# Performance work log

Hardware: AMD Instinct MI355X
Metric: run time of the kernel (lower is better)

The kernel has to match this reference:

```python
import jax, jax.numpy as jnp
import numpy as np

N = 8192
D = 256  # hidden_size = in_features = out_features
NEG_SLOPE = 0.01  # nn.LeakyReLU() default
MASK_VAL = -1e12


def setup_inputs() -> dict:
    key = jax.random.key(0)
    k1, k2, k3, k4 = jax.random.split(key, 4)
    x = jax.random.normal(k1, (N, D), dtype=jnp.float32)
    adj = jax.random.randint(k2, (N, N), 0, 2, dtype=jnp.int32)
    # kaiming_uniform_ style params (scaled random uniform)
    W = jax.random.normal(k3, (D, D), dtype=jnp.float32) * (1.0 / np.sqrt(D))
    a = jax.random.normal(k4, (2 * D, 1), dtype=jnp.float32) * (1.0 / np.sqrt(2 * D))
    return {"x": x, "adj": adj, "W": W, "a": a}


def reference(x, adj, W, a):
    # GraphAttentionLayer.forward (eval mode: dropout is identity)
    h = x @ W  # [N, D]
    # a_input[i,j] = concat(h_i, h_j); a_input @ a decomposes as:
    #   e[i,j] = h_i . a[:D] + h_j . a[D:]
    # identical math without materializing the [N, N, 2D] tensor.
    e_src = h @ a[:D, 0]  # [N]
    e_dst = h @ a[D:, 0]  # [N]
    e = e_src[:, None] + e_dst[None, :]  # [N, N]
    e = jnp.where(e > 0, e, NEG_SLOPE * e)  # LeakyReLU
    att_logits = jnp.where(adj > 0, e, MASK_VAL)
    attention = jax.nn.softmax(att_logits, axis=1)
    h_prime = attention @ h  # [N, D]
    return jax.nn.elu(h_prime)  # concat=True branch
```

## Files before the change

kernel.cpp:

```cpp
#include <hip/hip_runtime.h>

#define NN 8192
#define DD 256
#define JSPLIT 2
#define JCH (NN / JSPLIT)
#define NSTEP (JCH / 32)

typedef __attribute__((ext_vector_type(8))) short short8;
typedef __attribute__((ext_vector_type(4))) float f32x4;

__device__ __forceinline__ short f2bf(float x) {
    union { float f; unsigned u; } v; v.f = x;
    unsigned r = (v.u + 0x7FFFu + ((v.u >> 16) & 1u)) >> 16;
    return (short)r;
}
__device__ __forceinline__ float bf2f(short b) {
    union { float f; unsigned u; } v; v.u = ((unsigned)(unsigned short)b) << 16;
    return v.f;
}

__device__ __forceinline__ void barrier_keep_vmem() {
    asm volatile("s_waitcnt lgkmcnt(0)" ::: "memory");
    __builtin_amdgcn_s_barrier();
    asm volatile("" ::: "memory");
}

__global__ __launch_bounds__(256) void gat_prep(
    const float* __restrict__ x, const float* __restrict__ W,
    const float* __restrict__ a,
    short* __restrict__ hT, float* __restrict__ e_src, float* __restrict__ e_dst)
{
    __shared__ float x_s[32][260];
    __shared__ float W_s[2][16][256];
    const int t  = threadIdx.x;
    const int ib = blockIdx.x * 32;

    #pragma unroll
    for (int rep = 0; rep < 8; ++rep) {
        int fi = rep * 256 + t;
        int r  = fi >> 6;
        int c4 = (fi & 63) * 4;
        float4 v = *(const float4*)(x + (size_t)(ib + r) * DD + c4);
        *(float4*)&x_s[r][c4] = v;
    }
    float4 wp[4];
    #pragma unroll
    for (int q = 0; q < 4; ++q) {
        int fi = q * 256 + t;
        wp[q] = *(const float4*)(W + (size_t)(fi >> 6) * DD + (fi & 63) * 4);
    }
    barrier_keep_vmem();

    const int il = t >> 3;
    const int dg = (t & 7) * 4;
    f32x4 acc[8];
    #pragma unroll
    for (int m = 0; m < 8; ++m) acc[m] = (f32x4){0.f, 0.f, 0.f, 0.f};

    for (int kc = 0; kc < 16; ++kc) {
        const int b = kc & 1;
        #pragma unroll
        for (int q = 0; q < 4; ++q) {
            int fi = q * 256 + t;
            *(float4*)&W_s[b][fi >> 6][(fi & 63) * 4] = wp[q];
        }
        if (kc < 15) {
            #pragma unroll
            for (int q = 0; q < 4; ++q) {
                int fi = q * 256 + t;
                wp[q] = *(const float4*)(W + (size_t)((kc + 1) * 16 + (fi >> 6)) * DD + (fi & 63) * 4);
            }
        }
        barrier_keep_vmem();
        #pragma unroll
        for (int kl = 0; kl < 16; ++kl) {
            float xv = x_s[il][kc * 16 + kl];
            #pragma unroll
            for (int m = 0; m < 8; ++m) {
                float4 wv = *(const float4*)&W_s[b][kl][m * 32 + dg];
                acc[m].x += xv * wv.x; acc[m].y += xv * wv.y;
                acc[m].z += xv * wv.z; acc[m].w += xv * wv.w;
            }
        }
    }

    const int ig = ib + il;
    float p1 = 0.f, p2 = 0.f;
    #pragma unroll
    for (int m = 0; m < 8; ++m) {
        #pragma unroll
        for (int j = 0; j < 4; ++j) {
            int col = m * 32 + dg + j;
            float hv = acc[m][j];
            p1 += hv * a[col];
            p2 += hv * a[DD + col];
            hT[(size_t)col * NN + ig] = f2bf(hv);
        }
    }
    p1 += __shfl_xor(p1, 1); p1 += __shfl_xor(p1, 2); p1 += __shfl_xor(p1, 4);
    p2 += __shfl_xor(p2, 1); p2 += __shfl_xor(p2, 2); p2 += __shfl_xor(p2, 4);
    if ((t & 7) == 0) { e_src[ig] = p1; e_dst[ig] = p2; }
}

__global__ __launch_bounds__(512, 4) void gat_main(
    const int* __restrict__ adj, const short* __restrict__ hT,
    const float* __restrict__ e_src, const float* __restrict__ e_dst,
    float* __restrict__ num0, float* __restrict__ num1,
    float* __restrict__ den_part)
{
    __shared__ __align__(16) short B_s[2][256][40];
    __shared__ __align__(16) short w_s[2][32][40];

    const int t    = threadIdx.x;
    const int lane = t & 63;
    const int wid  = t >> 6;
    const int ibl  = (blockIdx.x >> 1) * 32;
    const int half = blockIdx.x & 1;
    const int jb   = half * JCH;

    const int irow = t >> 4;
    const int jc2  = (t & 15) * 2;
    const float es = e_src[ibl + irow];
    const int* adj_row = adj + (size_t)(ibl + irow) * NN + jb;
    const short* hrow = hT + (size_t)(t >> 1) * NN + jb + (t & 1) * 16;
    const float* edp = e_dst + jb;

    const int ihalf = wid & 1;
    const int dbase = (wid >> 1) * 64;
    const int arow  = lane & 15;
    const int kg8   = (lane >> 4) * 8;

    float dsum = 0.f;
    f32x4 acc0 = {0.f,0.f,0.f,0.f}, acc1 = acc0, acc2 = acc0, acc3 = acc0;

    int2   adA = *(const int2*)(adj_row + jc2);
    float2 edA = *(const float2*)(edp + jc2);
    int4   h0A = *(const int4*)(hrow);
    int4   h1A = *(const int4*)(hrow + 8);
    int2   adB = *(const int2*)(adj_row + 32 + jc2);
    float2 edB = *(const float2*)(edp + 32 + jc2);
    int4   h0B = *(const int4*)(hrow + 32);
    int4   h1B = *(const int4*)(hrow + 32 + 8);

#define MAIN_STEP(AD, ED, H0, H1, n)                                           \
    {                                                                          \
        const int c = (n) & 1;                                                 \
        float s0 = es + ED.x, s1 = es + ED.y;                                  \
        float l0 = s0 > 0.f ? s0 : 0.01f * s0;                                 \
        float l1 = s1 > 0.f ? s1 : 0.01f * s1;                                 \
        float w0 = AD.x > 0 ? __expf(l0) : 0.f;                                \
        float w1 = AD.y > 0 ? __expf(l1) : 0.f;                                \
        short b0 = f2bf(w0), b1 = f2bf(w1);                                    \
        dsum += bf2f(b0) + bf2f(b1);    \
        *(unsigned*)&w_s[c][irow][jc2] =                                       \
            (unsigned)(unsigned short)b0 | ((unsigned)(unsigned short)b1 << 16);\
        *(int4*)&B_s[c][t >> 1][(t & 1) * 16]     = H0;                        \
        *(int4*)&B_s[c][t >> 1][(t & 1) * 16 + 8] = H1;                        \
        int jn = (((n) + 2) & (NSTEP - 1)) * 32;         \
        AD = *(const int2*)(adj_row + jn + jc2);                               \
        ED = *(const float2*)(edp + jn + jc2);                                 \
        H0 = *(const int4*)(hrow + jn);                                        \
        H1 = *(const int4*)(hrow + jn + 8);                                    \
        barrier_keep_vmem();          \
        short8 af  = *(const short8*)&w_s[c][ihalf * 16 + arow][kg8];          \
        short8 bf0 = *(const short8*)&B_s[c][dbase +  0 + arow][kg8];          \
        short8 bf1 = *(const short8*)&B_s[c][dbase + 16 + arow][kg8];          \
        short8 bf2 = *(const short8*)&B_s[c][dbase + 32 + arow][kg8];          \
        short8 bf3 = *(const short8*)&B_s[c][dbase + 48 + arow][kg8];          \
        acc0 = __builtin_amdgcn_mfma_f32_16x16x32_bf16(af, bf0, acc0, 0, 0, 0);\
        acc1 = __builtin_amdgcn_mfma_f32_16x16x32_bf16(af, bf1, acc1, 0, 0, 0);\
        acc2 = __builtin_amdgcn_mfma_f32_16x16x32_bf16(af, bf2, acc2, 0, 0, 0);\
        acc3 = __builtin_amdgcn_mfma_f32_16x16x32_bf16(af, bf3, acc3, 0, 0, 0);\
    }

    for (int n = 0; n < NSTEP; n += 2) {
        MAIN_STEP(adA, edA, h0A, h1A, n)
        MAIN_STEP(adB, edB, h0B, h1B, n + 1)
    }
#undef MAIN_STEP

    dsum += __shfl_xor(dsum, 1);
    dsum += __shfl_xor(dsum, 2);
    dsum += __shfl_xor(dsum, 4);
    dsum += __shfl_xor(dsum, 8);
    if ((t & 15) == 0) den_part[half * NN + ibl + irow] = dsum;

    float* num = half ? num1 : num0;
    const int rbase = ihalf * 16 + (lane >> 4) * 4;
    #pragma unroll
    for (int r = 0; r < 4; ++r) {
        size_t o = (size_t)(ibl + rbase + r) * DD + dbase + arow;
        num[o]      = acc0[r];
        num[o + 16] = acc1[r];
        num[o + 32] = acc2[r];
        num[o + 48] = acc3[r];
    }
}

__global__ __launch_bounds__(256) void gat_epi(
    float* __restrict__ out, const float* __restrict__ num1,
    const float* __restrict__ den_part)
{
    int idx = blockIdx.x * 256 + threadIdx.x;
    int row = idx >> 6;
    float inv = 1.f / (den_part[row] + den_part[NN + row]);
    float4 p0 = ((const float4*)out)[idx];
    float4 p1 = ((const float4*)num1)[idx];
    float4 v;
    v.x = (p0.x + p1.x) * inv; v.x = v.x > 0.f ? v.x : expm1f(v.x);
    v.y = (p0.y + p1.y) * inv; v.y = v.y > 0.f ? v.y : expm1f(v.y);
    v.z = (p0.z + p1.z) * inv; v.z = v.z > 0.f ? v.z : expm1f(v.z);
    v.w = (p0.w + p1.w) * inv; v.w = v.w > 0.f ? v.w : expm1f(v.w);
    ((float4*)out)[idx] = v;
}

extern "C" void kernel_launch(void* const* d_in, const int* in_sizes, int n_in,
                              void* d_out, int out_size, void* d_ws, size_t ws_size,
                              hipStream_t stream) {
    const float* x   = (const float*)d_in[0];
    const int*   adj = (const int*)d_in[1];
    const float* W   = (const float*)d_in[2];
    const float* a   = (const float*)d_in[3];
    float* out = (float*)d_out;

    char* w0 = (char*)d_ws;
    short* hT   = (short*)w0;
    float* esrc = (float*)(w0 + (size_t)DD * NN * 2);
    float* edst = esrc + NN;
    float* den  = edst + NN;
    float* num1 = den + 2 * NN;

    gat_prep<<<dim3(NN / 32), dim3(256), 0, stream>>>(x, W, a, hT, esrc, edst);
    gat_main<<<dim3((NN / 32) * JSPLIT), dim3(512), 0, stream>>>(
        adj, hT, esrc, edst, out, num1, den);
    gat_epi<<<dim3(NN * DD / 4 / 256), dim3(256), 0, stream>>>(out, num1, den);
}
```

Before: 217.9 us.

## Load hT B-fragments directly from global into registers, dropping LDS staging

The main GAT kernel no longer stages the transposed h tile through shared memory. Each wave now owns 32 output columns and loads its MFMA B operands straight from global memory in fragment layout, prefetched one step ahead. Only the attention weights go through LDS, where each wave reads both 16-row A fragments. This removes the LDS writes and reads for B and shrinks shared memory per block. In exchange the global loads become per-lane 16-byte reads that stride across hT rows, which may coalesce worse.

```diff
diff --git a/kernel.cpp b/kernel.cpp
--- a/kernel.cpp
+++ b/kernel.cpp
@@ -108,7 +108,6 @@
     float* __restrict__ num0, float* __restrict__ num1,
     float* __restrict__ den_part)
 {
-    __shared__ __align__(16) short B_s[2][256][40];
     __shared__ __align__(16) short w_s[2][32][40];
 
     const int t    = threadIdx.x;
@@ -122,29 +121,29 @@
     const int jc2  = (t & 15) * 2;
     const float es = e_src[ibl + irow];
     const int* adj_row = adj + (size_t)(ibl + irow) * NN + jb;
-    const short* hrow = hT + (size_t)(t >> 1) * NN + jb + (t & 1) * 16;
     const float* edp = e_dst + jb;
 
-    const int ihalf = wid & 1;
-    const int dbase = (wid >> 1) * 64;
-    const int arow  = lane & 15;
-    const int kg8   = (lane >> 4) * 8;
+    const int cb   = wid * 32;
+    const int arow = lane & 15;
+    const int kg8  = (lane >> 4) * 8;
+    const short* hB = hT + (size_t)(cb + arow) * NN + jb + kg8;
 
     float dsum = 0.f;
-    f32x4 acc0 = {0.f,0.f,0.f,0.f}, acc1 = acc0, acc2 = acc0, acc3 = acc0;
+    f32x4 acc00 = {0.f,0.f,0.f,0.f}, acc01 = acc00, acc10 = acc00, acc11 = acc00;
 
     int2   adA = *(const int2*)(adj_row + jc2);
     float2 edA = *(const float2*)(edp + jc2);
-    int4   h0A = *(const int4*)(hrow);
-    int4   h1A = *(const int4*)(hrow + 8);
+    int4   b0A = *(const int4*)(hB);
+    int4   b1A = *(const int4*)(hB + 16 * NN);
     int2   adB = *(const int2*)(adj_row + 32 + jc2);
     float2 edB = *(const float2*)(edp + 32 + jc2);
-    int4   h0B = *(const int4*)(hrow + 32);
-    int4   h1B = *(const int4*)(hrow + 32 + 8);
-
-#define MAIN_STEP(AD, ED, H0, H1, n)                                           \
+    int4   b0B = *(const int4*)(hB + 32);
+    int4   b1B = *(const int4*)(hB + 16 * NN + 32);
+
+#define MAIN_STEP(AD, ED, B0, B1, n)                                           \
     {                                                                          \
         const int c = (n) & 1;                                                 \
+        int4 g0 = B0, g1 = B1;                       \
         float s0 = es + ED.x, s1 = es + ED.y;                                  \
         float l0 = s0 > 0.f ? s0 : 0.01f * s0;                                 \
         float l1 = s1 > 0.f ? s1 : 0.01f * s1;                                 \
@@ -154,28 +153,23 @@
         dsum += bf2f(b0) + bf2f(b1);    \
         *(unsigned*)&w_s[c][irow][jc2] =                                       \
             (unsigned)(unsigned short)b0 | ((unsigned)(unsigned short)b1 << 16);\
-        *(int4*)&B_s[c][t >> 1][(t & 1) * 16]     = H0;                        \
-        *(int4*)&B_s[c][t >> 1][(t & 1) * 16 + 8] = H1;                        \
         int jn = (((n) + 2) & (NSTEP - 1)) * 32;         \
         AD = *(const int2*)(adj_row + jn + jc2);                               \
         ED = *(const float2*)(edp + jn + jc2);                                 \
-        H0 = *(const int4*)(hrow + jn);                                        \
-        H1 = *(const int4*)(hrow + jn + 8);                                    \
+        B0 = *(const int4*)(hB + jn);                                          \
+        B1 = *(const int4*)(hB + 16 * NN + jn);                                \
         barrier_keep_vmem();          \
-        short8 af  = *(const short8*)&w_s[c][ihalf * 16 + arow][kg8];          \
-        short8 bf0 = *(const short8*)&B_s[c][dbase +  0 + arow][kg8];          \
-        short8 bf1 = *(const short8*)&B_s[c][dbase + 16 + arow][kg8];          \
-        short8 bf2 = *(const short8*)&B_s[c][dbase + 32 + arow][kg8];          \
-        short8 bf3 = *(const short8*)&B_s[c][dbase + 48 + arow][kg8];          \
-        acc0 = __builtin_amdgcn_mfma_f32_16x16x32_bf16(af, bf0, acc0, 0, 0, 0);\
-        acc1 = __builtin_amdgcn_mfma_f32_16x16x32_bf16(af, bf1, acc1, 0, 0, 0);\
-        acc2 = __builtin_amdgcn_mfma_f32_16x16x32_bf16(af, bf2, acc2, 0, 0, 0);\
-        acc3 = __builtin_amdgcn_mfma_f32_16x16x32_bf16(af, bf3, acc3, 0, 0, 0);\
+        short8 a0 = *(const short8*)&w_s[c][arow][kg8];                        \
+        short8 a1 = *(const short8*)&w_s[c][16 + arow][kg8];                   \
+        acc00 = __builtin_amdgcn_mfma_f32_16x16x32_bf16(a0, *(short8*)&g0, acc00, 0, 0, 0);\
+        acc01 = __builtin_amdgcn_mfma_f32_16x16x32_bf16(a0, *(short8*)&g1, acc01, 0, 0, 0);\
+        acc10 = __builtin_amdgcn_mfma_f32_16x16x32_bf16(a1, *(short8*)&g0, acc10, 0, 0, 0);\
+        acc11 = __builtin_amdgcn_mfma_f32_16x16x32_bf16(a1, *(short8*)&g1, acc11, 0, 0, 0);\
     }
 
     for (int n = 0; n < NSTEP; n += 2) {
-        MAIN_STEP(adA, edA, h0A, h1A, n)
-        MAIN_STEP(adB, edB, h0B, h1B, n + 1)
+        MAIN_STEP(adA, edA, b0A, b1A, n)
+        MAIN_STEP(adB, edB, b0B, b1B, n + 1)
     }
 #undef MAIN_STEP
 
@@ -186,14 +180,15 @@
     if ((t & 15) == 0) den_part[half * NN + ibl + irow] = dsum;
 
     float* num = half ? num1 : num0;
-    const int rbase = ihalf * 16 + (lane >> 4) * 4;
+    const int r4 = (lane >> 4) * 4;
     #pragma unroll
     for (int r = 0; r < 4; ++r) {
-        size_t o = (size_t)(ibl + rbase + r) * DD + dbase + arow;
-        num[o]      = acc0[r];
-        num[o + 16] = acc1[r];
-        num[o + 32] = acc2[r];
-        num[o + 48] = acc3[r];
+        size_t o0 = (size_t)(ibl + r4 + r) * DD + cb + arow;
+        size_t o1 = (size_t)(ibl + 16 + r4 + r) * DD + cb + arow;
+        num[o0]      = acc00[r];
+        num[o0 + 16] = acc01[r];
+        num[o1]      = acc10[r];
+        num[o1 + 16] = acc11[r];
     }
 }
 
```

After: 225.3 us. 3.4% more time.
